# Performance work log

Measured on AMD Instinct MI355X. Metric: run time of the kernel, lower is better.

The kernel has to match this reference:

```python
import jax, jax.numpy as jnp
import numpy as np

N = 8192
H = 256
R = 3

def setup_inputs() -> dict:
    key = jax.random.key(0)
    k1, k2, k3 = jax.random.split(key, 3)
    x = jax.random.normal(k1, (N, H), dtype=jnp.float32)
    # dense adjacency per relation, stacked: [R, N, N]
    adjs = jax.random.uniform(k2, (R, N, N), dtype=jnp.float32)
    # glorot-uniform-scaled relation weights: [R, H, H]
    limit = np.sqrt(6.0 / (H + H)).astype(np.float32)
    W = jax.random.uniform(k3, (R, H, H), dtype=jnp.float32, minval=-limit, maxval=limit)
    return {"x": x, "adjs": adjs, "W": W}

def reference(x, adjs, W) -> jnp.ndarray:
    # xw[r] = x @ W[r]  -> [R, N, H]
    xw = jnp.einsum('nh,rhk->rnk', x, W)
    # out = sum_r adjs[r] @ xw[r]  -> [N, H]
    out = jnp.einsum('rmn,rnk->mk', adjs, xw)
    return out
```

## Files before the change

kernel.cpp:

```cpp
#include <hip/hip_runtime.h>
#include <hip/hip_bf16.h>

#define NN 8192
#define HH 256
#define RR 3

#define BM 128
#define BK 64
#define SPLIT 4
#define KSLICE (NN / SPLIT)

typedef __attribute__((ext_vector_type(8))) short     bf16x8;
typedef __attribute__((ext_vector_type(4))) float     f32x4;
typedef __attribute__((ext_vector_type(4))) unsigned short u16x4;
typedef __attribute__((ext_vector_type(8))) unsigned short u16x8;

__device__ __forceinline__ unsigned short f2bf(float f) {
    unsigned int u = __builtin_bit_cast(unsigned int, f);
    u += 0x7FFF + ((u >> 16) & 1);
    return (unsigned short)(u >> 16);
}

__global__ __launch_bounds__(256) void xw_kernel(
    const float* __restrict__ x, const float* __restrict__ W,
    unsigned short* __restrict__ xwt)
{
    const int r  = blockIdx.y;
    const int k0 = blockIdx.x * 16;
    const int c  = threadIdx.x;

    __shared__ float xs[16][HH];

    for (int idx = threadIdx.x; idx < 16 * (HH / 4); idx += 256) {
        const int i  = idx >> 6;
        const int h4 = idx & 63;
        ((f32x4*)xs[i])[h4] = ((const f32x4*)(x + (size_t)(k0 + i) * HH))[h4];
    }
    __syncthreads();

    float acc[16];
#pragma unroll
    for (int i = 0; i < 16; ++i) acc[i] = 0.f;

    const float* Wr = W + (size_t)r * HH * HH;
    for (int h = 0; h < HH; h += 8) {
        float w0 = Wr[(h + 0) * HH + c];
        float w1 = Wr[(h + 1) * HH + c];
        float w2 = Wr[(h + 2) * HH + c];
        float w3 = Wr[(h + 3) * HH + c];
        float w4 = Wr[(h + 4) * HH + c];
        float w5 = Wr[(h + 5) * HH + c];
        float w6 = Wr[(h + 6) * HH + c];
        float w7 = Wr[(h + 7) * HH + c];
#pragma unroll
        for (int i = 0; i < 16; ++i) {
            const f32x4 a = *(const f32x4*)&xs[i][h];
            const f32x4 b = *(const f32x4*)&xs[i][h + 4];
            acc[i] += a.x * w0 + a.y * w1 + a.z * w2 + a.w * w3
                    + b.x * w4 + b.y * w5 + b.z * w6 + b.w * w7;
        }
    }

    u16x8 lo, hi;
#pragma unroll
    for (int i = 0; i < 8; ++i) { lo[i] = f2bf(acc[i]); hi[i] = f2bf(acc[i + 8]); }
    u16x8* dst = (u16x8*)(xwt + ((size_t)r * HH + c) * NN + k0);
    dst[0] = lo;
    dst[1] = hi;
}

__global__ __launch_bounds__(512) void rgcn_spmm(
    const float* __restrict__ adjs, const unsigned short* __restrict__ xwt,
    float* __restrict__ out)
{
    __shared__ unsigned short As[BM * BK];
    __shared__ unsigned short Bs[HH * BK];

    const int id  = blockIdx.x + gridDim.x * blockIdx.y;
    const int swz = (id & 7) * 96 + (id >> 3);
    const int bx  = swz & 63;
    const int by  = swz >> 6;

    const int m0    = bx * BM;
    const int r     = by / SPLIT;
    const int slice = by % SPLIT;
    const int k0    = slice * KSLICE;

    const float*          A = adjs + (size_t)r * NN * NN;
    const unsigned short* B = xwt  + (size_t)r * HH * NN;

    const int tid  = threadIdx.x;
    const int lane = tid & 63;
    const int wave = tid >> 6;
    const int wm   = wave >> 2;
    const int wn   = wave & 3;

    f32x4 acc[4][4];
#pragma unroll
    for (int m = 0; m < 4; ++m)
#pragma unroll
        for (int n = 0; n < 4; ++n) acc[m][n] = (f32x4){0.f, 0.f, 0.f, 0.f};

    for (int kk = 0; kk < KSLICE; kk += BK) {
        const int kbase = k0 + kk;

#pragma unroll
        for (int p = 0; p < 4; ++p) {
            const int row = p * 32 + (tid >> 4);
            const int col = (tid & 15) << 2;
            const f32x4 v = *(const f32x4*)(A + (size_t)(m0 + row) * NN + kbase + col);
            u16x4 b4;
            b4.x = f2bf(v.x); b4.y = f2bf(v.y); b4.z = f2bf(v.z); b4.w = f2bf(v.w);
            const int byte = (col << 1) ^ ((row & 7) << 4);
            *(u16x4*)((char*)(As + row * BK) + byte) = b4;
        }
#pragma unroll
        for (int p = 0; p < 4; ++p) {
            const int crow  = p * 64 + (tid >> 3);
            const int chunk = tid & 7;
            const u16x8 v = *(const u16x8*)(B + (size_t)crow * NN + kbase + chunk * 8);
            const int byte = ((chunk << 4) ^ ((crow & 7) << 4));
            *(u16x8*)((char*)(Bs + crow * BK) + byte) = v;
        }
        __syncthreads();

#pragma unroll
        for (int ks = 0; ks < 2; ++ks) {
            bf16x8 af[4], bfr[4];
#pragma unroll
            for (int m = 0; m < 4; ++m) {
                const int row  = wm * 64 + m * 16 + (lane & 15);
                const int col  = ks * 32 + (lane >> 4) * 8;
                const int byte = (col << 1) ^ ((row & 7) << 4);
                af[m] = *(const bf16x8*)((const char*)(As + row * BK) + byte);
            }
#pragma unroll
            for (int n = 0; n < 4; ++n) {
                const int crow = wn * 64 + n * 16 + (lane & 15);
                const int col  = ks * 32 + (lane >> 4) * 8;
                const int byte = (col << 1) ^ ((crow & 7) << 4);
                bfr[n] = *(const bf16x8*)((const char*)(Bs + crow * BK) + byte);
            }
#pragma unroll
            for (int m = 0; m < 4; ++m)
#pragma unroll
                for (int n = 0; n < 4; ++n)
                    acc[m][n] = __builtin_amdgcn_mfma_f32_16x16x32_bf16(
                        af[m], bfr[n], acc[m][n], 0, 0, 0);
        }
        __syncthreads();
    }

#pragma unroll
    for (int m = 0; m < 4; ++m) {
#pragma unroll
        for (int n = 0; n < 4; ++n) {
            const int colb = wn * 64 + n * 16 + (lane & 15);
            const int rowb = m0 + wm * 64 + m * 16 + (lane >> 4) * 4;
#pragma unroll
            for (int j = 0; j < 4; ++j)
                atomicAdd(out + (size_t)(rowb + j) * HH + colb, acc[m][n][j]);
        }
    }
}

extern "C" void kernel_launch(void* const* d_in, const int* in_sizes, int n_in,
                              void* d_out, int out_size, void* d_ws, size_t ws_size,
                              hipStream_t stream)
{
    const float* x    = (const float*)d_in[0];
    const float* adjs = (const float*)d_in[1];
    const float* W    = (const float*)d_in[2];
    float* out = (float*)d_out;
    unsigned short* xwt = (unsigned short*)d_ws;

    hipMemsetAsync(d_out, 0, (size_t)out_size * sizeof(float), stream);

    dim3 gA(NN / 16, RR);
    xw_kernel<<<gA, 256, 0, stream>>>(x, W, xwt);

    dim3 gB(NN / BM, RR * SPLIT);
    rgcn_spmm<<<gB, 512, 0, stream>>>(adjs, xwt, out);
}
```

Measured before the change: 1.150 ms.

## Double-buffer SpMM loop, fold relations into K, pre-tile xw, replace atomics with partials

The main kernel now folds the three relations into one long K loop per block, with BM reduced to 64 and 256 threads. It double-buffers shared memory: the next A tile is prefetched into registers and the next B tile is loaded straight into LDS with global_load_lds while the current tile is computed. The xw kernel now writes xw in a pre-tiled, pre-swizzled layout so B tiles can be copied contiguously. Float atomics into the output are replaced by per-split partial buffers and a separate reduce kernel, which adds partial-buffer traffic and one extra launch.

```diff
diff --git a/kernel.cpp b/kernel.cpp
--- a/kernel.cpp
+++ b/kernel.cpp
@@ -5,15 +5,19 @@
 #define HH 256
 #define RR 3
 
-#define BM 128
+#define BM 64
 #define BK 64
 #define SPLIT 4
 #define KSLICE (NN / SPLIT)
-
-typedef __attribute__((ext_vector_type(8))) short     bf16x8;
-typedef __attribute__((ext_vector_type(4))) float     f32x4;
+#define NT (RR * KSLICE / BK)
+
+typedef __attribute__((ext_vector_type(8))) short          bf16x8;
+typedef __attribute__((ext_vector_type(4))) float          f32x4;
 typedef __attribute__((ext_vector_type(4))) unsigned short u16x4;
 typedef __attribute__((ext_vector_type(8))) unsigned short u16x8;
+
+typedef const __attribute__((address_space(1))) unsigned int gbl_u32;
+typedef __attribute__((address_space(3)))       unsigned int lds_u32;
 
 __device__ __forceinline__ unsigned short f2bf(float f) {
     unsigned int u = __builtin_bit_cast(unsigned int, f);
@@ -64,36 +68,32 @@
     u16x8 lo, hi;
 #pragma unroll
     for (int i = 0; i < 8; ++i) { lo[i] = f2bf(acc[i]); hi[i] = f2bf(acc[i + 8]); }
-    u16x8* dst = (u16x8*)(xwt + ((size_t)r * HH + c) * NN + k0);
-    dst[0] = lo;
-    dst[1] = hi;
-}
-
-__global__ __launch_bounds__(512) void rgcn_spmm(
+
+    const int  kt   = k0 >> 6;
+    const int  ks0b = (k0 & 63) * 2;
+    const int  s    = (c & 7) << 4;
+    char* tb = (char*)xwt + (((size_t)r * 128 + kt) << 15) + c * 128;
+    *(u16x8*)(tb + (ks0b ^ s))        = lo;
+    *(u16x8*)(tb + ((ks0b + 16) ^ s)) = hi;
+}
+
+__global__ __launch_bounds__(256, 2) void rgcn_spmm(
     const float* __restrict__ adjs, const unsigned short* __restrict__ xwt,
-    float* __restrict__ out)
-{
-    __shared__ unsigned short As[BM * BK];
-    __shared__ unsigned short Bs[HH * BK];
-
-    const int id  = blockIdx.x + gridDim.x * blockIdx.y;
-    const int swz = (id & 7) * 96 + (id >> 3);
-    const int bx  = swz & 63;
-    const int by  = swz >> 6;
-
-    const int m0    = bx * BM;
-    const int r     = by / SPLIT;
-    const int slice = by % SPLIT;
+    float* __restrict__ part)
+{
+    __shared__ unsigned short As[2][BM * BK];
+    __shared__ unsigned short Bs[2][HH * BK];
+
+    const int id    = blockIdx.x;
+    const int swz   = (id & 7) * 64 + (id >> 3);
+    const int slice = swz >> 7;
+    const int mtile = swz & 127;
+    const int m0    = mtile * BM;
     const int k0    = slice * KSLICE;
-
-    const float*          A = adjs + (size_t)r * NN * NN;
-    const unsigned short* B = xwt  + (size_t)r * HH * NN;
 
     const int tid  = threadIdx.x;
     const int lane = tid & 63;
-    const int wave = tid >> 6;
-    const int wm   = wave >> 2;
-    const int wn   = wave & 3;
+    const int wn   = tid >> 6;
 
     f32x4 acc[4][4];
 #pragma unroll
@@ -101,45 +101,61 @@
 #pragma unroll
         for (int n = 0; n < 4; ++n) acc[m][n] = (f32x4){0.f, 0.f, 0.f, 0.f};
 
-    for (int kk = 0; kk < KSLICE; kk += BK) {
-        const int kbase = k0 + kk;
-
+    auto a_issue = [&](int t, f32x4* areg) {
+        const int r  = t >> 5;
+        const int kb = k0 + ((t & 31) << 6);
+        const float* A = adjs + (size_t)r * NN * NN + (size_t)m0 * NN + kb;
 #pragma unroll
         for (int p = 0; p < 4; ++p) {
-            const int row = p * 32 + (tid >> 4);
-            const int col = (tid & 15) << 2;
-            const f32x4 v = *(const f32x4*)(A + (size_t)(m0 + row) * NN + kbase + col);
+            const int idx  = p * 256 + tid;
+            const int row  = idx >> 4;
+            const int col4 = idx & 15;
+            areg[p] = *(const f32x4*)(A + (size_t)row * NN + col4 * 4);
+        }
+    };
+    auto b_issue = [&](int t, int buf) {
+        const int r  = t >> 5;
+        const int kt = (k0 >> 6) + (t & 31);
+        const char* src = (const char*)xwt + (((size_t)r * 128 + kt) << 15);
+        char* dst = (char*)Bs[buf];
+#pragma unroll
+        for (int j = 0; j < 8; ++j) {
+            const int off = (j * 4 + wn) * 1024;
+            __builtin_amdgcn_global_load_lds(
+                (gbl_u32*)(src + off + lane * 16),
+                (lds_u32*)(dst + off), 16, 0, 0);
+        }
+    };
+    auto a_commit = [&](const f32x4* areg, int buf) {
+        char* dst = (char*)As[buf];
+#pragma unroll
+        for (int p = 0; p < 4; ++p) {
+            const int idx  = p * 256 + tid;
+            const int row  = idx >> 4;
+            const int col4 = idx & 15;
             u16x4 b4;
-            b4.x = f2bf(v.x); b4.y = f2bf(v.y); b4.z = f2bf(v.z); b4.w = f2bf(v.w);
-            const int byte = (col << 1) ^ ((row & 7) << 4);
-            *(u16x4*)((char*)(As + row * BK) + byte) = b4;
-        }
-#pragma unroll
-        for (int p = 0; p < 4; ++p) {
-            const int crow  = p * 64 + (tid >> 3);
-            const int chunk = tid & 7;
-            const u16x8 v = *(const u16x8*)(B + (size_t)crow * NN + kbase + chunk * 8);
-            const int byte = ((chunk << 4) ^ ((crow & 7) << 4));
-            *(u16x8*)((char*)(Bs + crow * BK) + byte) = v;
-        }
-        __syncthreads();
-
+            b4.x = f2bf(areg[p].x); b4.y = f2bf(areg[p].y);
+            b4.z = f2bf(areg[p].z); b4.w = f2bf(areg[p].w);
+            const int byte = (col4 * 8) ^ ((row & 7) << 4);
+            *(u16x4*)(dst + row * 128 + byte) = b4;
+        }
+    };
+    auto compute = [&](int buf) {
 #pragma unroll
         for (int ks = 0; ks < 2; ++ks) {
             bf16x8 af[4], bfr[4];
+            const int colb = ks * 64 + (lane >> 4) * 16;
 #pragma unroll
             for (int m = 0; m < 4; ++m) {
-                const int row  = wm * 64 + m * 16 + (lane & 15);
-                const int col  = ks * 32 + (lane >> 4) * 8;
-                const int byte = (col << 1) ^ ((row & 7) << 4);
-                af[m] = *(const bf16x8*)((const char*)(As + row * BK) + byte);
+                const int row = m * 16 + (lane & 15);
+                af[m] = *(const bf16x8*)((const char*)As[buf] + row * 128
+                         + (colb ^ ((row & 7) << 4)));
             }
 #pragma unroll
             for (int n = 0; n < 4; ++n) {
                 const int crow = wn * 64 + n * 16 + (lane & 15);
-                const int col  = ks * 32 + (lane >> 4) * 8;
-                const int byte = (col << 1) ^ ((crow & 7) << 4);
-                bfr[n] = *(const bf16x8*)((const char*)(Bs + crow * BK) + byte);
+                bfr[n] = *(const bf16x8*)((const char*)Bs[buf] + crow * 128
+                         + (colb ^ ((crow & 7) << 4)));
             }
 #pragma unroll
             for (int m = 0; m < 4; ++m)
@@ -148,20 +164,50 @@
                     acc[m][n] = __builtin_amdgcn_mfma_f32_16x16x32_bf16(
                         af[m], bfr[n], acc[m][n], 0, 0, 0);
         }
+    };
+
+    {
+        f32x4 areg[4];
+        a_issue(0, areg);
+        b_issue(0, 0);
+        a_commit(areg, 0);
+    }
+    __syncthreads();
+
+    int cur = 0;
+    for (int t = 0; t < NT - 1; ++t) {
+        f32x4 areg[4];
+        a_issue(t + 1, areg);
+        b_issue(t + 1, cur ^ 1);
+        compute(cur);
+        a_commit(areg, cur ^ 1);
         __syncthreads();
-    }
-
+        cur ^= 1;
+    }
+    compute(cur);
+
+    float* dst = part + (size_t)slice * NN * HH;
 #pragma unroll
     for (int m = 0; m < 4; ++m) {
+        const int rowb = m0 + m * 16 + (lane >> 4) * 4;
 #pragma unroll
         for (int n = 0; n < 4; ++n) {
             const int colb = wn * 64 + n * 16 + (lane & 15);
-            const int rowb = m0 + wm * 64 + m * 16 + (lane >> 4) * 4;
 #pragma unroll
             for (int j = 0; j < 4; ++j)
-                atomicAdd(out + (size_t)(rowb + j) * HH + colb, acc[m][n][j]);
-        }
-    }
+                dst[(size_t)(rowb + j) * HH + colb] = acc[m][n][j];
+        }
+    }
+}
+
+__global__ __launch_bounds__(256) void reduce_kernel(
+    const float* __restrict__ part, float* __restrict__ out)
+{
+    const size_t S  = (size_t)NN * HH / 4;
+    const size_t i  = (size_t)blockIdx.x * 256 + threadIdx.x;
+    const f32x4* p  = (const f32x4*)part;
+    f32x4 v = p[i] + p[i + S] + p[i + 2 * S] + p[i + 3 * S];
+    ((f32x4*)out)[i] = v;
 }
 
 extern "C" void kernel_launch(void* const* d_in, const int* in_sizes, int n_in,
@@ -172,13 +218,14 @@
     const float* adjs = (const float*)d_in[1];
     const float* W    = (const float*)d_in[2];
     float* out = (float*)d_out;
+
     unsigned short* xwt = (unsigned short*)d_ws;
-
-    hipMemsetAsync(d_out, 0, (size_t)out_size * sizeof(float), stream);
+    float* part = (float*)((char*)d_ws + ((size_t)RR * 128 << 15));
 
     dim3 gA(NN / 16, RR);
     xw_kernel<<<gA, 256, 0, stream>>>(x, W, xwt);
 
-    dim3 gB(NN / BM, RR * SPLIT);
-    rgcn_spmm<<<gB, 512, 0, stream>>>(adjs, xwt, out);
-}
+    rgcn_spmm<<<NN / BM * SPLIT, 256, 0, stream>>>(adjs, xwt, part);
+
+    reduce_kernel<<<(NN * HH / 4) / 256, 256, 0, stream>>>(part, out);
+}
```

New measurement: 1.165 ms. About the same (+1.4%).
